# Optimization experiments

Hardware: AMD Instinct MI355X
Metric: run time of the kernel (lower is better)

Reference implementation:

```python
import jax, jax.numpy as jnp
import numpy as np

N_NODES = 50000
N_EDGES = 800000
D_IN = 128
HIDDEN = [128, 128]
D_OUT = 64


def setup_inputs() -> dict:
    key = jax.random.key(0)
    ks = jax.random.split(key, 12)
    x = jax.random.normal(ks[0], (N_NODES, D_IN), dtype=jnp.float32)
    edge_index = jax.random.randint(ks[1], (2, N_EDGES), 0, N_NODES, dtype=jnp.int64)
    # SAGEConv params: lin_l acts on aggregated neighbors (has bias), lin_r on root
    def lin(k, fan_in, fan_out):
        s = 1.0 / np.sqrt(fan_in)
        return jax.random.uniform(k, (fan_in, fan_out), jnp.float32, -s, s)
    dims = [D_IN] + HIDDEN
    inp = {"x": x, "edge_index": edge_index}
    for i in range(len(HIDDEN)):
        inp[f"Wl{i}"] = lin(ks[2 + 3 * i], dims[i], dims[i + 1])
        inp[f"Wr{i}"] = lin(ks[3 + 3 * i], dims[i], dims[i + 1])
        inp[f"b{i}"] = jnp.zeros((dims[i + 1],), jnp.float32)
    inp["Wfc"] = lin(ks[10], HIDDEN[-1], D_OUT)
    inp["bfc"] = jnp.zeros((D_OUT,), jnp.float32)
    return inp


def _sage_conv(x, src, dst, n, Wl, Wr, b, deg_inv):
    # mean-aggregate source features into destination nodes
    agg = jax.ops.segment_sum(x[src], dst, num_segments=n) * deg_inv[:, None]
    return agg @ Wl + x @ Wr + b


def reference(x, edge_index, Wl0, Wr0, b0, Wl1, Wr1, b1, Wfc, bfc):
    src, dst = edge_index[0], edge_index[1]
    n = x.shape[0]
    deg = jax.ops.segment_sum(jnp.ones((src.shape[0],), x.dtype), dst, num_segments=n)
    deg_inv = 1.0 / jnp.maximum(deg, 1.0)
    h = jax.nn.relu(_sage_conv(x, src, dst, n, Wl0, Wr0, b0, deg_inv))
    # dropout p=0 / eval mode -> identity
    h = jax.nn.relu(_sage_conv(h, src, dst, n, Wl1, Wr1, b1, deg_inv))
    return h @ Wfc + bfc
```

## Files before the change

kernel.cpp:

```cpp
#include <hip/hip_runtime.h>
#include <hip/hip_bf16.h>

#define NN 50000
#define NE 800000
#define D 128
#define DOUT 64
#define PAD 64
#define BSH 8
#define NBUCK 196
#define CHUNK 4096
#define NBINB 196
#define SEGC 64
#define BPITCH 68
#define EPITCH 72
#define N8 (NN * D / 8)

#define PACKB2 9
#define CASTB2 128

typedef __attribute__((ext_vector_type(8))) short short8;
typedef __attribute__((ext_vector_type(4))) float float4v;


__device__ inline unsigned short f2bf(float f) {
    union { float f; unsigned int i; } c; c.f = f;
    unsigned int u = c.i;
    return (unsigned short)((u + 0x7fffu + ((u >> 16) & 1u)) >> 16);
}
__device__ inline float bflo(unsigned int u) {
    union { unsigned int i; float f; } c; c.i = u << 16; return c.f;
}
__device__ inline float bfhi(unsigned int u) {
    union { unsigned int i; float f; } c; c.i = u & 0xffff0000u; return c.f;
}


__global__ void bin_edges(const int* __restrict__ src, const int* __restrict__ dst,
                          unsigned int* __restrict__ binned, int* __restrict__ cnts) {
    __shared__ int cnt[NBUCK];
    __shared__ __align__(16) unsigned int buf[NBUCK * BPITCH];
    int blk = blockIdx.x;
    int tid = threadIdx.x;
    for (int b = tid; b < NBUCK; b += 256) cnt[b] = 0;
    __syncthreads();
    int base = blk * CHUNK;
#pragma unroll
    for (int i = 0; i < 16; ++i) {
        int e = base + i * 256 + tid;
        if (e < NE) {
            unsigned int d = (unsigned int)dst[e];
            unsigned int s = (unsigned int)src[e];
            int q = d >> BSH;
            int slot = atomicAdd(&cnt[q], 1);
            if (slot < SEGC)
                buf[q * BPITCH + slot] = (d << 16) | s;
        }
    }
    __syncthreads();
    for (int b = tid; b < NBUCK; b += 256)
        cnts[blk * NBUCK + b] = (cnt[b] < SEGC) ? cnt[b] : SEGC;
    uint4* ob = (uint4*)(binned + (size_t)blk * NBUCK * SEGC);
    for (int j = tid; j < NBUCK * (SEGC / 4); j += 256) {
        int q2 = j >> 4;
        int part = j & 15;
        int c = cnt[q2] < SEGC ? cnt[q2] : SEGC;
        if (part * 4 < c)
            ob[j] = *(const uint4*)&buf[q2 * BPITCH + part * 4];
    }
}


struct Stage2Args {
    const unsigned int* binned;
    const int* cnts;
    unsigned short* eidx_pad;
    int* cursor;
    const float* W[5];
    unsigned short* P[5];
    const float* x;
    unsigned short* xb;
    unsigned short* zrow;
};

__global__ __launch_bounds__(1024)
void stage2(Stage2Args args) {
    int blk = blockIdx.x;
    int tid = threadIdx.x;
    if (blk < NBUCK) {
        __shared__ int cur[256];
        __shared__ int segc[NBINB];
        __shared__ __align__(16) unsigned short eix[256 * EPITCH];
        int q = blk;
        if (tid < 256) cur[tid] = 0;
        for (int s = tid; s < NBINB; s += 1024) segc[s] = args.cnts[(size_t)s * NBUCK + q];
        __syncthreads();
        for (int i4 = tid; i4 < NBINB * (SEGC / 4); i4 += 1024) {
            int seg = i4 >> 4;
            int kb = (i4 & 15) << 2;
            int c = segc[seg];
            if (kb < c) {
                uint4 r4 = *(const uint4*)(args.binned + ((size_t)seg * NBUCK + q) * SEGC + kb);
#define PLACE(rv, ok)                                                     \
                if (ok) {                                                 \
                    int dl = ((rv) >> 16) & 255;                          \
                    int sl = atomicAdd(&cur[dl], 1);                      \
                    if (sl < PAD) eix[dl * EPITCH + sl] = (unsigned short)((rv) & 0xffffu); \
                }
                PLACE(r4.x, true)
                PLACE(r4.y, kb + 1 < c)
                PLACE(r4.z, kb + 2 < c)
                PLACE(r4.w, kb + 3 < c)
#undef PLACE
            }
        }
        __syncthreads();
        int nbase = q << BSH;
        int nlim = NN - nbase;
        if (nlim > 256) nlim = 256;
        uint4* op = (uint4*)(args.eidx_pad + (size_t)nbase * PAD);
        for (int j = tid; j < 2048; j += 1024) {
            int node = j >> 3;
            if (node < nlim)
                op[j] = *(const uint4*)&eix[node * EPITCH + (j & 7) * 8];
        }
        if (tid < 256) {
            int node = nbase + tid;
            if (node < NN) args.cursor[node] = (cur[tid] < PAD) ? cur[tid] : PAD;
        }
    } else if (blk < NBUCK + PACKB2) {
        int idx = (blk - NBUCK) * 1024 + tid;
        if (idx < 9216) {
            const float* W;
            unsigned short* P;
            int COLS, local;
            if (idx < 4 * 2048) {
                int wsel = idx >> 11;
                W = args.W[wsel]; P = args.P[wsel]; COLS = 128; local = idx & 2047;
            } else {
                W = args.W[4]; P = args.P[4]; COLS = 64; local = idx - 4 * 2048;
            }
            int CT = COLS >> 4;
            int lane = local & 63;
            int fi = local >> 6;
            int ct = fi % CT;
            int kstep = fi / CT;
            int krow = kstep * 32 + (lane >> 4) * 8;
            int col = ct * 16 + (lane & 15);
            unsigned short v[8];
#pragma unroll
            for (int j = 0; j < 8; ++j) v[j] = f2bf(W[(size_t)(krow + j) * COLS + col]);
            unsigned int w0 = v[0] | ((unsigned int)v[1] << 16);
            unsigned int w1 = v[2] | ((unsigned int)v[3] << 16);
            unsigned int w2 = v[4] | ((unsigned int)v[5] << 16);
            unsigned int w3 = v[6] | ((unsigned int)v[7] << 16);
            *(uint4*)(P + (size_t)local * 8) = make_uint4(w0, w1, w2, w3);
        }
        if (blk == NBUCK && tid < 16)
            *(uint4*)(args.zrow + (size_t)tid * 8) = make_uint4(0, 0, 0, 0);
    } else {
        int stride = CASTB2 * 1024;
        for (int i = (blk - NBUCK - PACKB2) * 1024 + tid; i < N8; i += stride) {
            const float4* p = (const float4*)args.x + (size_t)i * 2;
            float4 a = p[0], bb = p[1];
            unsigned int w0 = f2bf(a.x) | ((unsigned int)f2bf(a.y) << 16);
            unsigned int w1 = f2bf(a.z) | ((unsigned int)f2bf(a.w) << 16);
            unsigned int w2 = f2bf(bb.x) | ((unsigned int)f2bf(bb.y) << 16);
            unsigned int w3 = f2bf(bb.z) | ((unsigned int)f2bf(bb.w) << 16);
            *(uint4*)(args.xb + (size_t)i * 8) = make_uint4(w0, w1, w2, w3);
        }
    }
}


template <bool FUSEFC>
__global__ __launch_bounds__(256, 4)
void fused_layer(const unsigned short* __restrict__ feat,
                 const int* __restrict__ cursor, const unsigned short* __restrict__ eidx_pad,
                 const unsigned short* __restrict__ zrow,
                 const unsigned short* __restrict__ Pl, const unsigned short* __restrict__ Pr,
                 const float* __restrict__ bias,
                 const unsigned short* __restrict__ Pfc, const float* __restrict__ bfc,
                 unsigned short* __restrict__ outb, float* __restrict__ outf, int n) {
    __shared__ __align__(16) unsigned short As[64][136];

    int tid = threadIdx.x;
    int row0 = blockIdx.x * 64;

    {
        int g = tid >> 4;
        int l = tid & 15;
        int nbase = row0 + g * 4;
        int4 dv = *(const int4*)(cursor + nbase);
        const unsigned short* rbase = eidx_pad + (size_t)nbase * PAD;
        uint4 ia = *(const uint4*)(rbase);
        uint4 ib = *(const uint4*)(rbase + 8);
#pragma unroll
        for (int nn = 0; nn < 4; ++nn) {
            int r = g * 4 + nn;
            int node = nbase + nn;
            uint4 ca = ia, cb = ib;
            if (nn < 3) {
                ia = *(const uint4*)(rbase + (nn + 1) * PAD);
                ib = *(const uint4*)(rbase + (nn + 1) * PAD + 8);
            }
            int deg = 0;
            if (node < n) {
                deg = ((const int*)&dv)[nn];
                if (deg > PAD) deg = PAD;
            }
            float di = 1.0f / (float)(deg > 1 ? deg : 1);
            float acc[8] = {0.f, 0.f, 0.f, 0.f, 0.f, 0.f, 0.f, 0.f};
            {
                int id[16];
                id[0] = ca.x & 0xffff;  id[1] = ca.x >> 16;
                id[2] = ca.y & 0xffff;  id[3] = ca.y >> 16;
                id[4] = ca.z & 0xffff;  id[5] = ca.z >> 16;
                id[6] = ca.w & 0xffff;  id[7] = ca.w >> 16;
                id[8] = cb.x & 0xffff;  id[9] = cb.x >> 16;
                id[10] = cb.y & 0xffff; id[11] = cb.y >> 16;
                id[12] = cb.z & 0xffff; id[13] = cb.z >> 16;
                id[14] = cb.w & 0xffff; id[15] = cb.w >> 16;
                uint4 v[16];
#pragma unroll
                for (int k = 0; k < 16; ++k) {
                    const unsigned short* sp = (k < deg) ? (feat + (size_t)id[k] * D) : zrow;
                    v[k] = *(const uint4*)(sp + l * 8);
                }
#pragma unroll
                for (int k = 0; k < 16; ++k) {
                    acc[0] += bflo(v[k].x); acc[1] += bfhi(v[k].x);
                    acc[2] += bflo(v[k].y); acc[3] += bfhi(v[k].y);
                    acc[4] += bflo(v[k].z); acc[5] += bfhi(v[k].z);
                    acc[6] += bflo(v[k].w); acc[7] += bfhi(v[k].w);
                }
                const unsigned short* rowp = rbase + nn * PAD;
                int p = 16;
                while (p < deg) {
                    uint4 iv = *(const uint4*)(rowp + p);
                    int jd[8];
                    jd[0] = iv.x & 0xffff; jd[1] = iv.x >> 16;
                    jd[2] = iv.y & 0xffff; jd[3] = iv.y >> 16;
                    jd[4] = iv.z & 0xffff; jd[5] = iv.z >> 16;
                    jd[6] = iv.w & 0xffff; jd[7] = iv.w >> 16;
                    uint4 w[8];
#pragma unroll
                    for (int k = 0; k < 8; ++k) {
                        const unsigned short* sp = (p + k < deg) ? (feat + (size_t)jd[k] * D) : zrow;
                        w[k] = *(const uint4*)(sp + l * 8);
                    }
#pragma unroll
                    for (int k = 0; k < 8; ++k) {
                        acc[0] += bflo(w[k].x); acc[1] += bfhi(w[k].x);
                        acc[2] += bflo(w[k].y); acc[3] += bfhi(w[k].y);
                        acc[4] += bflo(w[k].z); acc[5] += bfhi(w[k].z);
                        acc[6] += bflo(w[k].w); acc[7] += bfhi(w[k].w);
                    }
                    p += 8;
                }
            }
            unsigned int w0 = f2bf(acc[0] * di) | ((unsigned int)f2bf(acc[1] * di) << 16);
            unsigned int w1 = f2bf(acc[2] * di) | ((unsigned int)f2bf(acc[3] * di) << 16);
            unsigned int w2 = f2bf(acc[4] * di) | ((unsigned int)f2bf(acc[5] * di) << 16);
            unsigned int w3 = f2bf(acc[6] * di) | ((unsigned int)f2bf(acc[7] * di) << 16);
            *(uint4*)&As[r][l * 8] = make_uint4(w0, w1, w2, w3);
        }
    }

    int wave = tid >> 6;
    int lane = tid & 63;
    int m16 = lane & 15;
    int quad = lane >> 4;
    int rt0 = (wave & 1) * 32;
    int ctb = (wave >> 1) * 4;

    float4v acc[2][4];
#pragma unroll
    for (int t = 0; t < 2; ++t)
#pragma unroll
        for (int c = 0; c < 4; ++c) acc[t][c] = (float4v){0.f, 0.f, 0.f, 0.f};

#pragma unroll
    for (int ks = 0; ks < 4; ++ks) {
        short8 xf[2];
#pragma unroll
        for (int t = 0; t < 2; ++t) {
            int row = row0 + rt0 + t * 16 + m16;
            short8 z = {0, 0, 0, 0, 0, 0, 0, 0};
            xf[t] = (row < n) ? *(const short8*)(feat + (size_t)row * D + ks * 32 + quad * 8) : z;
        }
#pragma unroll
        for (int c = 0; c < 4; ++c) {
            short8 bf = *(const short8*)(Pr + ((size_t)((ks * 8 + ctb + c) * 64 + lane)) * 8);
#pragma unroll
            for (int t = 0; t < 2; ++t)
                acc[t][c] = __builtin_amdgcn_mfma_f32_16x16x32_bf16(xf[t], bf, acc[t][c], 0, 0, 0);
        }
    }

    __syncthreads();

#pragma unroll
    for (int ks = 0; ks < 4; ++ks) {
        short8 af[2];
#pragma unroll
        for (int t = 0; t < 2; ++t)
            af[t] = *(const short8*)&As[rt0 + t * 16 + m16][ks * 32 + quad * 8];
#pragma unroll
        for (int c = 0; c < 4; ++c) {
            short8 bf = *(const short8*)(Pl + ((size_t)((ks * 8 + ctb + c) * 64 + lane)) * 8);
#pragma unroll
            for (int t = 0; t < 2; ++t)
                acc[t][c] = __builtin_amdgcn_mfma_f32_16x16x32_bf16(af[t], bf, acc[t][c], 0, 0, 0);
        }
    }

    if (!FUSEFC) {
#pragma unroll
        for (int t = 0; t < 2; ++t) {
#pragma unroll
            for (int c = 0; c < 4; ++c) {
                int col = (ctb + c) * 16 + m16;
                float bv = bias[col];
#pragma unroll
                for (int i = 0; i < 4; ++i) {
                    int row = row0 + rt0 + t * 16 + quad * 4 + i;
                    if (row < n)
                        outb[(size_t)row * D + col] = f2bf(fmaxf(acc[t][c][i] + bv, 0.f));
                }
            }
        }
    } else {
        __syncthreads();
#pragma unroll
        for (int t = 0; t < 2; ++t) {
#pragma unroll
            for (int c = 0; c < 4; ++c) {
                int col = (ctb + c) * 16 + m16;
                float bv = bias[col];
#pragma unroll
                for (int i = 0; i < 4; ++i) {
                    int row = rt0 + t * 16 + quad * 4 + i;
                    As[row][col] = f2bf(fmaxf(acc[t][c][i] + bv, 0.f));
                }
            }
        }
        __syncthreads();

        int ctbF = (wave >> 1) * 2;
        float4v acc2[2][2];
#pragma unroll
        for (int t = 0; t < 2; ++t)
#pragma unroll
            for (int c = 0; c < 2; ++c) acc2[t][c] = (float4v){0.f, 0.f, 0.f, 0.f};
#pragma unroll
        for (int ks = 0; ks < 4; ++ks) {
            short8 hf[2];
#pragma unroll
            for (int t = 0; t < 2; ++t)
                hf[t] = *(const short8*)&As[rt0 + t * 16 + m16][ks * 32 + quad * 8];
#pragma unroll
            for (int c = 0; c < 2; ++c) {
                short8 bf = *(const short8*)(Pfc + ((size_t)((ks * 4 + ctbF + c) * 64 + lane)) * 8);
#pragma unroll
                for (int t = 0; t < 2; ++t)
                    acc2[t][c] = __builtin_amdgcn_mfma_f32_16x16x32_bf16(hf[t], bf, acc2[t][c], 0, 0, 0);
            }
        }
#pragma unroll
        for (int t = 0; t < 2; ++t) {
#pragma unroll
            for (int c = 0; c < 2; ++c) {
                int col = (ctbF + c) * 16 + m16;
                float bv = bfc[col];
#pragma unroll
                for (int i = 0; i < 4; ++i) {
                    int row = row0 + rt0 + t * 16 + quad * 4 + i;
                    if (row < n)
                        outf[(size_t)row * DOUT + col] = acc2[t][c][i] + bv;
                }
            }
        }
    }
}


extern "C" void kernel_launch(void* const* d_in, const int* in_sizes, int n_in,
                              void* d_out, int out_size, void* d_ws, size_t ws_size,
                              hipStream_t stream) {
    const float* x   = (const float*)d_in[0];
    const int*   ei  = (const int*)d_in[1];
    const float* Wl0 = (const float*)d_in[2];
    const float* Wr0 = (const float*)d_in[3];
    const float* b0  = (const float*)d_in[4];
    const float* Wl1 = (const float*)d_in[5];
    const float* Wr1 = (const float*)d_in[6];
    const float* b1  = (const float*)d_in[7];
    const float* Wfc = (const float*)d_in[8];
    const float* bfc = (const float*)d_in[9];
    float* out = (float*)d_out;

    const int* src = ei;
    const int* dst = ei + NE;

    char* p = (char*)d_ws;
    auto carve = [&](size_t bytes) {
        char* q = p;
        p += (bytes + 255) & ~(size_t)255;
        return q;
    };
    int*            cursor   = (int*)carve(NN * sizeof(int));
    int*            cnts     = (int*)carve((size_t)NBINB * NBUCK * sizeof(int));
    unsigned short* zrow     = (unsigned short*)carve(256);
    unsigned int*   binned   = (unsigned int*)carve((size_t)NBINB * NBUCK * SEGC * 4);
    unsigned short* eidx_pad = (unsigned short*)carve((size_t)NN * PAD * 2);
    unsigned short* xb   = (unsigned short*)carve((size_t)NN * D * 2);
    unsigned short* h0b  = (unsigned short*)carve((size_t)NN * D * 2);
    unsigned short* Wl0p = (unsigned short*)carve(D * D * 2);
    unsigned short* Wr0p = (unsigned short*)carve(D * D * 2);
    unsigned short* Wl1p = (unsigned short*)carve(D * D * 2);
    unsigned short* Wr1p = (unsigned short*)carve(D * D * 2);
    unsigned short* Wfcp = (unsigned short*)carve(D * DOUT * 2);

    bin_edges<<<NBINB, 256, 0, stream>>>(src, dst, binned, cnts);

    Stage2Args s2;
    s2.binned = binned; s2.cnts = cnts;
    s2.eidx_pad = eidx_pad; s2.cursor = cursor;
    s2.W[0] = Wl0; s2.W[1] = Wr0; s2.W[2] = Wl1; s2.W[3] = Wr1; s2.W[4] = Wfc;
    s2.P[0] = Wl0p; s2.P[1] = Wr0p; s2.P[2] = Wl1p; s2.P[3] = Wr1p; s2.P[4] = Wfcp;
    s2.x = x; s2.xb = xb; s2.zrow = zrow;
    stage2<<<NBUCK + PACKB2 + CASTB2, 1024, 0, stream>>>(s2);

    const int GB = (NN + 63) / 64;

    fused_layer<false><<<GB, 256, 0, stream>>>(xb, cursor, eidx_pad, zrow, Wl0p, Wr0p, b0,
                                               nullptr, nullptr, h0b, nullptr, NN);
    fused_layer<true><<<GB, 256, 0, stream>>>(h0b, cursor, eidx_pad, zrow, Wl1p, Wr1p, b1,
                                              Wfcp, bfc, nullptr, out, NN);
}
```

Measured before the change: 183.4 us.

## Merge edge binning and scatter prep into one cooperative kernel with grid sync

Edge binning, weight packing, x-to-bf16 casting and the per-bucket scatter are now one cooperative launch. A grid-wide barrier separates the binning phase from the scatter phase, replacing a kernel boundary. Binning moves to 1024-thread blocks, and x casting moves into the first phase so it runs alongside binning. If the cooperative launch fails, it falls back to two ordinary kernels. This saves a launch and its gap, but the 392-block grid must fit co-resident at 1024 threads with large shared memory, and the grid sync itself has a cost.

Measured after the change: 386.6 us. 2.11x slower.

```diff
diff --git a/kernel.cpp b/kernel.cpp
--- a/kernel.cpp
+++ b/kernel.cpp
@@ -1,5 +1,8 @@
 #include <hip/hip_runtime.h>
 #include <hip/hip_bf16.h>
+#include <hip/hip_cooperative_groups.h>
+
+namespace cg = cooperative_groups;
 
 #define NN 50000
 #define NE 800000
@@ -15,8 +18,9 @@
 #define EPITCH 72
 #define N8 (NN * D / 8)
 
-#define PACKB2 9
-#define CASTB2 128
+#define PACKB 9
+#define CASTB 187
+#define PGRID (NBINB + PACKB + CASTB)
 
 typedef __attribute__((ext_vector_type(8))) short short8;
 typedef __attribute__((ext_vector_type(4))) float float4v;
@@ -35,44 +39,11 @@
 }
 
 
-__global__ void bin_edges(const int* __restrict__ src, const int* __restrict__ dst,
-                          unsigned int* __restrict__ binned, int* __restrict__ cnts) {
-    __shared__ int cnt[NBUCK];
-    __shared__ __align__(16) unsigned int buf[NBUCK * BPITCH];
-    int blk = blockIdx.x;
-    int tid = threadIdx.x;
-    for (int b = tid; b < NBUCK; b += 256) cnt[b] = 0;
-    __syncthreads();
-    int base = blk * CHUNK;
-#pragma unroll
-    for (int i = 0; i < 16; ++i) {
-        int e = base + i * 256 + tid;
-        if (e < NE) {
-            unsigned int d = (unsigned int)dst[e];
-            unsigned int s = (unsigned int)src[e];
-            int q = d >> BSH;
-            int slot = atomicAdd(&cnt[q], 1);
-            if (slot < SEGC)
-                buf[q * BPITCH + slot] = (d << 16) | s;
-        }
-    }
-    __syncthreads();
-    for (int b = tid; b < NBUCK; b += 256)
-        cnts[blk * NBUCK + b] = (cnt[b] < SEGC) ? cnt[b] : SEGC;
-    uint4* ob = (uint4*)(binned + (size_t)blk * NBUCK * SEGC);
-    for (int j = tid; j < NBUCK * (SEGC / 4); j += 256) {
-        int q2 = j >> 4;
-        int part = j & 15;
-        int c = cnt[q2] < SEGC ? cnt[q2] : SEGC;
-        if (part * 4 < c)
-            ob[j] = *(const uint4*)&buf[q2 * BPITCH + part * 4];
-    }
-}
-
-
-struct Stage2Args {
-    const unsigned int* binned;
-    const int* cnts;
+struct PrepArgs {
+    const int* src;
+    const int* dst;
+    unsigned int* binned;
+    int* cnts;
     unsigned short* eidx_pad;
     int* cursor;
     const float* W[5];
@@ -82,93 +53,168 @@
     unsigned short* zrow;
 };
 
-__global__ __launch_bounds__(1024)
-void stage2(Stage2Args args) {
+
+__device__ inline void bin_body(const PrepArgs& a, int blk, int tid,
+                                int* cnt, unsigned int* buf) {
+    for (int b = tid; b < NBUCK; b += 1024) cnt[b] = 0;
+    __syncthreads();
+    int base = blk * CHUNK;
+#pragma unroll
+    for (int i = 0; i < 4; ++i) {
+        int e = base + i * 1024 + tid;
+        if (e < NE) {
+            unsigned int d = (unsigned int)a.dst[e];
+            unsigned int s = (unsigned int)a.src[e];
+            int q = d >> BSH;
+            int slot = atomicAdd(&cnt[q], 1);
+            if (slot < SEGC)
+                buf[q * BPITCH + slot] = (d << 16) | s;
+        }
+    }
+    __syncthreads();
+    for (int b = tid; b < NBUCK; b += 1024)
+        a.cnts[blk * NBUCK + b] = (cnt[b] < SEGC) ? cnt[b] : SEGC;
+    uint4* ob = (uint4*)(a.binned + (size_t)blk * NBUCK * SEGC);
+    for (int j = tid; j < NBUCK * (SEGC / 4); j += 1024) {
+        int q2 = j >> 4;
+        int part = j & 15;
+        int c = cnt[q2] < SEGC ? cnt[q2] : SEGC;
+        if (part * 4 < c)
+            ob[j] = *(const uint4*)&buf[q2 * BPITCH + part * 4];
+    }
+}
+
+__device__ inline void scatter_body(const PrepArgs& a, int q, int tid,
+                                    int* cur, int* segc, unsigned short* eix) {
+    if (tid < 256) cur[tid] = 0;
+    for (int s = tid; s < NBINB; s += 1024) segc[s] = a.cnts[(size_t)s * NBUCK + q];
+    __syncthreads();
+    for (int i4 = tid; i4 < NBINB * (SEGC / 4); i4 += 1024) {
+        int seg = i4 >> 4;
+        int kb = (i4 & 15) << 2;
+        int c = segc[seg];
+        if (kb < c) {
+            uint4 r4 = *(const uint4*)(a.binned + ((size_t)seg * NBUCK + q) * SEGC + kb);
+#define PLACE(rv, ok)                                                     \
+            if (ok) {                                                     \
+                int dl = ((rv) >> 16) & 255;                              \
+                int sl = atomicAdd(&cur[dl], 1);                          \
+                if (sl < PAD) eix[dl * EPITCH + sl] = (unsigned short)((rv) & 0xffffu); \
+            }
+            PLACE(r4.x, true)
+            PLACE(r4.y, kb + 1 < c)
+            PLACE(r4.z, kb + 2 < c)
+            PLACE(r4.w, kb + 3 < c)
+#undef PLACE
+        }
+    }
+    __syncthreads();
+    int nbase = q << BSH;
+    int nlim = NN - nbase;
+    if (nlim > 256) nlim = 256;
+    uint4* op = (uint4*)(a.eidx_pad + (size_t)nbase * PAD);
+    for (int j = tid; j < 2048; j += 1024) {
+        int node = j >> 3;
+        if (node < nlim)
+            op[j] = *(const uint4*)&eix[node * EPITCH + (j & 7) * 8];
+    }
+    if (tid < 256) {
+        int node = nbase + tid;
+        if (node < NN) a.cursor[node] = (cur[tid] < PAD) ? cur[tid] : PAD;
+    }
+}
+
+__device__ inline void pack_body(const PrepArgs& a, int idx) {
+    const float* W;
+    unsigned short* P;
+    int COLS, local;
+    if (idx < 4 * 2048) {
+        int wsel = idx >> 11;
+        W = a.W[wsel]; P = a.P[wsel]; COLS = 128; local = idx & 2047;
+    } else {
+        W = a.W[4]; P = a.P[4]; COLS = 64; local = idx - 4 * 2048;
+    }
+    int CT = COLS >> 4;
+    int lane = local & 63;
+    int fi = local >> 6;
+    int ct = fi % CT;
+    int kstep = fi / CT;
+    int krow = kstep * 32 + (lane >> 4) * 8;
+    int col = ct * 16 + (lane & 15);
+    unsigned short v[8];
+#pragma unroll
+    for (int j = 0; j < 8; ++j) v[j] = f2bf(W[(size_t)(krow + j) * COLS + col]);
+    unsigned int w0 = v[0] | ((unsigned int)v[1] << 16);
+    unsigned int w1 = v[2] | ((unsigned int)v[3] << 16);
+    unsigned int w2 = v[4] | ((unsigned int)v[5] << 16);
+    unsigned int w3 = v[6] | ((unsigned int)v[7] << 16);
+    *(uint4*)(P + (size_t)local * 8) = make_uint4(w0, w1, w2, w3);
+}
+
+__device__ inline void cast_body(const PrepArgs& a, int start, int stride) {
+    for (int i = start; i < N8; i += stride) {
+        const float4* p = (const float4*)a.x + (size_t)i * 2;
+        float4 av = p[0], bb = p[1];
+        unsigned int w0 = f2bf(av.x) | ((unsigned int)f2bf(av.y) << 16);
+        unsigned int w1 = f2bf(av.z) | ((unsigned int)f2bf(av.w) << 16);
+        unsigned int w2 = f2bf(bb.x) | ((unsigned int)f2bf(bb.y) << 16);
+        unsigned int w3 = f2bf(bb.z) | ((unsigned int)f2bf(bb.w) << 16);
+        *(uint4*)(a.xb + (size_t)i * 8) = make_uint4(w0, w1, w2, w3);
+    }
+}
+
+
+__global__ __launch_bounds__(1024, 8)
+void prep_all(PrepArgs a) {
+    __shared__ __align__(16) unsigned char smem[1024 + NBUCK * BPITCH * 4];
     int blk = blockIdx.x;
     int tid = threadIdx.x;
+    if (blk < NBINB) {
+        int* cnt = (int*)smem;
+        unsigned int* buf = (unsigned int*)(smem + 1024);
+        bin_body(a, blk, tid, cnt, buf);
+    } else if (blk < NBINB + PACKB) {
+        int idx = (blk - NBINB) * 1024 + tid;
+        if (idx < 9216) pack_body(a, idx);
+        if (blk == NBINB && tid < 16)
+            *(uint4*)(a.zrow + (size_t)tid * 8) = make_uint4(0, 0, 0, 0);
+    } else {
+        cast_body(a, (blk - NBINB - PACKB) * 1024 + tid, CASTB * 1024);
+    }
+    __threadfence();
+    cg::this_grid().sync();
     if (blk < NBUCK) {
-        __shared__ int cur[256];
-        __shared__ int segc[NBINB];
-        __shared__ __align__(16) unsigned short eix[256 * EPITCH];
-        int q = blk;
-        if (tid < 256) cur[tid] = 0;
-        for (int s = tid; s < NBINB; s += 1024) segc[s] = args.cnts[(size_t)s * NBUCK + q];
-        __syncthreads();
-        for (int i4 = tid; i4 < NBINB * (SEGC / 4); i4 += 1024) {
-            int seg = i4 >> 4;
-            int kb = (i4 & 15) << 2;
-            int c = segc[seg];
-            if (kb < c) {
-                uint4 r4 = *(const uint4*)(args.binned + ((size_t)seg * NBUCK + q) * SEGC + kb);
-#define PLACE(rv, ok)                                                     \
-                if (ok) {                                                 \
-                    int dl = ((rv) >> 16) & 255;                          \
-                    int sl = atomicAdd(&cur[dl], 1);                      \
-                    if (sl < PAD) eix[dl * EPITCH + sl] = (unsigned short)((rv) & 0xffffu); \
-                }
-                PLACE(r4.x, true)
-                PLACE(r4.y, kb + 1 < c)
-                PLACE(r4.z, kb + 2 < c)
-                PLACE(r4.w, kb + 3 < c)
-#undef PLACE
-            }
-        }
-        __syncthreads();
-        int nbase = q << BSH;
-        int nlim = NN - nbase;
-        if (nlim > 256) nlim = 256;
-        uint4* op = (uint4*)(args.eidx_pad + (size_t)nbase * PAD);
-        for (int j = tid; j < 2048; j += 1024) {
-            int node = j >> 3;
-            if (node < nlim)
-                op[j] = *(const uint4*)&eix[node * EPITCH + (j & 7) * 8];
-        }
-        if (tid < 256) {
-            int node = nbase + tid;
-            if (node < NN) args.cursor[node] = (cur[tid] < PAD) ? cur[tid] : PAD;
-        }
-    } else if (blk < NBUCK + PACKB2) {
-        int idx = (blk - NBUCK) * 1024 + tid;
-        if (idx < 9216) {
-            const float* W;
-            unsigned short* P;
-            int COLS, local;
-            if (idx < 4 * 2048) {
-                int wsel = idx >> 11;
-                W = args.W[wsel]; P = args.P[wsel]; COLS = 128; local = idx & 2047;
-            } else {
-                W = args.W[4]; P = args.P[4]; COLS = 64; local = idx - 4 * 2048;
-            }
-            int CT = COLS >> 4;
-            int lane = local & 63;
-            int fi = local >> 6;
-            int ct = fi % CT;
-            int kstep = fi / CT;
-            int krow = kstep * 32 + (lane >> 4) * 8;
-            int col = ct * 16 + (lane & 15);
-            unsigned short v[8];
-#pragma unroll
-            for (int j = 0; j < 8; ++j) v[j] = f2bf(W[(size_t)(krow + j) * COLS + col]);
-            unsigned int w0 = v[0] | ((unsigned int)v[1] << 16);
-            unsigned int w1 = v[2] | ((unsigned int)v[3] << 16);
-            unsigned int w2 = v[4] | ((unsigned int)v[5] << 16);
-            unsigned int w3 = v[6] | ((unsigned int)v[7] << 16);
-            *(uint4*)(P + (size_t)local * 8) = make_uint4(w0, w1, w2, w3);
-        }
-        if (blk == NBUCK && tid < 16)
-            *(uint4*)(args.zrow + (size_t)tid * 8) = make_uint4(0, 0, 0, 0);
+        int* cur = (int*)smem;
+        int* segc = (int*)(smem + 1024);
+        unsigned short* eix = (unsigned short*)(smem + 2048);
+        scatter_body(a, blk, tid, cur, segc, eix);
+    }
+}
+
+
+__global__ __launch_bounds__(1024, 8)
+void prep_a(PrepArgs a) {
+    __shared__ __align__(16) unsigned char smem[1024 + NBUCK * BPITCH * 4];
+    int blk = blockIdx.x;
+    int tid = threadIdx.x;
+    if (blk < NBINB) {
+        bin_body(a, blk, tid, (int*)smem, (unsigned int*)(smem + 1024));
+    } else if (blk < NBINB + PACKB) {
+        int idx = (blk - NBINB) * 1024 + tid;
+        if (idx < 9216) pack_body(a, idx);
+        if (blk == NBINB && tid < 16)
+            *(uint4*)(a.zrow + (size_t)tid * 8) = make_uint4(0, 0, 0, 0);
     } else {
-        int stride = CASTB2 * 1024;
-        for (int i = (blk - NBUCK - PACKB2) * 1024 + tid; i < N8; i += stride) {
-            const float4* p = (const float4*)args.x + (size_t)i * 2;
-            float4 a = p[0], bb = p[1];
-            unsigned int w0 = f2bf(a.x) | ((unsigned int)f2bf(a.y) << 16);
-            unsigned int w1 = f2bf(a.z) | ((unsigned int)f2bf(a.w) << 16);
-            unsigned int w2 = f2bf(bb.x) | ((unsigned int)f2bf(bb.y) << 16);
-            unsigned int w3 = f2bf(bb.z) | ((unsigned int)f2bf(bb.w) << 16);
-            *(uint4*)(args.xb + (size_t)i * 8) = make_uint4(w0, w1, w2, w3);
-        }
-    }
+        cast_body(a, (blk - NBINB - PACKB) * 1024 + tid, CASTB * 1024);
+    }
+}
+
+__global__ __launch_bounds__(1024, 8)
+void prep_b(PrepArgs a) {
+    __shared__ int cur[256];
+    __shared__ int segc[NBINB];
+    __shared__ __align__(16) unsigned short eix[256 * EPITCH];
+    scatter_body(a, blockIdx.x, threadIdx.x, cur, segc, eix);
 }
 
 
@@ -421,15 +467,22 @@
     unsigned short* Wr1p = (unsigned short*)carve(D * D * 2);
     unsigned short* Wfcp = (unsigned short*)carve(D * DOUT * 2);
 
-    bin_edges<<<NBINB, 256, 0, stream>>>(src, dst, binned, cnts);
-
-    Stage2Args s2;
-    s2.binned = binned; s2.cnts = cnts;
-    s2.eidx_pad = eidx_pad; s2.cursor = cursor;
-    s2.W[0] = Wl0; s2.W[1] = Wr0; s2.W[2] = Wl1; s2.W[3] = Wr1; s2.W[4] = Wfc;
-    s2.P[0] = Wl0p; s2.P[1] = Wr0p; s2.P[2] = Wl1p; s2.P[3] = Wr1p; s2.P[4] = Wfcp;
-    s2.x = x; s2.xb = xb; s2.zrow = zrow;
-    stage2<<<NBUCK + PACKB2 + CASTB2, 1024, 0, stream>>>(s2);
+    PrepArgs pa;
+    pa.src = src; pa.dst = dst;
+    pa.binned = binned; pa.cnts = cnts;
+    pa.eidx_pad = eidx_pad; pa.cursor = cursor;
+    pa.W[0] = Wl0; pa.W[1] = Wr0; pa.W[2] = Wl1; pa.W[3] = Wr1; pa.W[4] = Wfc;
+    pa.P[0] = Wl0p; pa.P[1] = Wr0p; pa.P[2] = Wl1p; pa.P[3] = Wr1p; pa.P[4] = Wfcp;
+    pa.x = x; pa.xb = xb; pa.zrow = zrow;
+
+    void* kargs[] = {(void*)&pa};
+    hipError_t ce = hipLaunchCooperativeKernel((const void*)prep_all, dim3(PGRID),
+                                               dim3(1024), kargs, 0, stream);
+    if (ce != hipSuccess) {
+        (void)hipGetLastError();
+        prep_a<<<PGRID, 1024, 0, stream>>>(pa);
+        prep_b<<<NBUCK, 1024, 0, stream>>>(pa);
+    }
 
     const int GB = (NN + 63) / 64;
 
```
